# Performance work log

Measured on AMD Instinct MI355X. Metric: run time of the kernel, lower is better.

## Reference

```python
import jax
import jax.numpy as jnp
from jax import lax
import numpy as np

N_PRE = 1024
N_POST = 2048
SEQ_LEN = 4096
DECAY = 0.9   # leak factor per timestep
V_TH = 1.0    # firing threshold


def setup_inputs() -> dict:
    key = jax.random.key(0)
    k1, k2 = jax.random.split(key)
    stim = (jax.random.uniform(k1, (N_PRE, SEQ_LEN), dtype=jnp.float32) < 0.1).astype(jnp.float32)  # sparse input spikes
    weights = jax.random.normal(k2, (N_POST, N_PRE), dtype=jnp.float32) * 0.05
    return {"stim": stim, "weights": weights}


def reference(stim, weights):
    # Synaptic currents for all timesteps at once: cal_post_input(stim[:, i]) == weights @ stim[:, i]
    currents = jnp.einsum("np,pt->nt", weights, stim)  # [n_post, T]

    def lif_step(v, i_t):
        # leaky integrate
        v = v * DECAY + i_t
        # fire
        s = (v >= V_TH).astype(v.dtype)
        # reset to 0 where spiked
        v_next = jnp.where(s > 0, jnp.zeros_like(v), v)
        return v_next, (s, v_next)

    v0 = jnp.zeros((N_POST,), dtype=stim.dtype)
    _, (spikes_t, v_t) = lax.scan(lif_step, v0, currents.T)  # scanned over T
    # transpose back to [n_post, T] to match spike_times / v buffers
    return spikes_t.T, v_t.T
```

## Files before the change

kernel.cpp:

```cpp
#include <hip/hip_runtime.h>

#define N_PRE 1024
#define N_POST 2048
#define SEQ_LEN 4096

#define KSPLIT 512

__device__ __forceinline__ float opaque(float x) {
  asm volatile("" : "+v"(x));
  return x;
}

__device__ __forceinline__ float load_dyn(const void* p, size_t idx, bool isbf) {
  if (isbf) {
    const unsigned short b = ((const unsigned short*)p)[idx];
    return __uint_as_float(((unsigned int)b) << 16);
  }
  return ((const float*)p)[idx];
}

__device__ __forceinline__ int sniff_flags(const void* W, const void* S, int tid,
                                           int* flags_sh) {
  if (tid < 64) {
    const unsigned short* uw = (const unsigned short*)W;
    const float f = fabsf(__uint_as_float(((unsigned int)uw[tid * 2]) << 16));
    const bool big = !(f < 64.f);
    const unsigned long long wb = __ballot(big);
    const unsigned short* us = (const unsigned short*)S;
    int hit = 0;
    for (int j = 0; j < 64; ++j) hit |= (us[tid * 128 + 2 * j] == 0x3F80u) ? 1 : 0;
    const unsigned long long sb = __ballot(hit != 0);
    if (tid == 0) *flags_sh = ((wb == 0ull) ? 1 : 0) | ((sb != 0ull) ? 2 : 0);
  }
  __syncthreads();
  return *flags_sh;
}

__global__ __launch_bounds__(256) void snn_wt_build(const void* __restrict__ W,
                                                    const void* __restrict__ S,
                                                    float* __restrict__ WT) {
  __shared__ float tile[64][65];
  __shared__ int flags_sh;
  const int tid = threadIdx.x;
  const int fl = sniff_flags(W, S, tid, &flags_sh);
  const bool w_bf = (fl & 1) != 0;
  const int k0 = blockIdx.x * 64;
  const int nn0 = blockIdx.y * 64;
  {
    const int r = tid >> 2;
    const int cq = tid & 3;
    if (!w_bf) {
      const float* Wf = (const float*)W;
#pragma unroll
      for (int p = 0; p < 4; ++p) {
        const int c = cq * 16 + p * 4;
        const float4 va = *(const float4*)&Wf[(size_t)(nn0 + r) * N_PRE + k0 + c];
        tile[c + 0][r] = va.x; tile[c + 1][r] = va.y;
        tile[c + 2][r] = va.z; tile[c + 3][r] = va.w;
      }
    } else {
#pragma unroll
      for (int p = 0; p < 4; ++p)
#pragma unroll
        for (int j = 0; j < 4; ++j) {
          const int c = cq * 16 + p * 4 + j;
          tile[c][r] = load_dyn(W, (size_t)(nn0 + r) * N_PRE + k0 + c, true);
        }
    }
  }
  __syncthreads();
  {
    const int kr = tid >> 2;
    const int nq = tid & 3;
#pragma unroll
    for (int p = 0; p < 4; ++p) {
      const int c = nq * 16 + p * 4;
      float4 o;
      o.x = tile[kr][c + 0]; o.y = tile[kr][c + 1];
      o.z = tile[kr][c + 2]; o.w = tile[kr][c + 3];
      *(float4*)&WT[(size_t)(k0 + kr) * N_POST + nn0 + c] = o;
    }
  }
}

__global__ __launch_bounds__(64) void snn_mask_build(const void* __restrict__ W,
                                                     const void* __restrict__ S,
                                                     unsigned char* __restrict__ MT) {
  __shared__ int flags_sh;
  const int tid = threadIdx.x;
  const int fl = sniff_flags(W, S, tid, &flags_sh);
  const bool s_bf = (fl & 2) != 0;
  const int tb = blockIdx.x;
  unsigned wrd[4] = {0u, 0u, 0u, 0u};
#pragma unroll
  for (int kk = 0; kk < 16; ++kk) {
    const int k = tid * 16 + kk;
    unsigned byte = 0;
    if (s_bf) {
      const unsigned short* Sb = (const unsigned short*)S;
      const uint4 u = *(const uint4*)&Sb[(size_t)k * SEQ_LEN + tb * 8];
      byte |= (((u.x & 0x7FFFu) != 0u) ? 1u : 0u) << 0;
      byte |= (((u.x & 0x7FFF0000u) != 0u) ? 1u : 0u) << 1;
      byte |= (((u.y & 0x7FFFu) != 0u) ? 1u : 0u) << 2;
      byte |= (((u.y & 0x7FFF0000u) != 0u) ? 1u : 0u) << 3;
      byte |= (((u.z & 0x7FFFu) != 0u) ? 1u : 0u) << 4;
      byte |= (((u.z & 0x7FFF0000u) != 0u) ? 1u : 0u) << 5;
      byte |= (((u.w & 0x7FFFu) != 0u) ? 1u : 0u) << 6;
      byte |= (((u.w & 0x7FFF0000u) != 0u) ? 1u : 0u) << 7;
    } else {
      const float* Sf = (const float*)S;
      const size_t base = (size_t)k * SEQ_LEN + tb * 8;
      const float4 f0 = *(const float4*)&Sf[base];
      const float4 f1 = *(const float4*)&Sf[base + 4];
      byte |= ((f0.x != 0.0f) ? 1u : 0u) << 0;
      byte |= ((f0.y != 0.0f) ? 1u : 0u) << 1;
      byte |= ((f0.z != 0.0f) ? 1u : 0u) << 2;
      byte |= ((f0.w != 0.0f) ? 1u : 0u) << 3;
      byte |= ((f1.x != 0.0f) ? 1u : 0u) << 4;
      byte |= ((f1.y != 0.0f) ? 1u : 0u) << 5;
      byte |= ((f1.z != 0.0f) ? 1u : 0u) << 6;
      byte |= ((f1.w != 0.0f) ? 1u : 0u) << 7;
    }
    wrd[kk >> 2] |= byte << ((kk & 3) * 8);
  }
  *(uint4*)&MT[(size_t)tb * N_PRE + tid * 16] =
      make_uint4(wrd[0], wrd[1], wrd[2], wrd[3]);
}

__global__ __launch_bounds__(64) void snn_list_build(const unsigned char* __restrict__ MT,
                                                     unsigned short* __restrict__ lists,
                                                     int* __restrict__ lens,
                                                     int* __restrict__ splits) {
  const int t = blockIdx.x;
  const int l = threadIdx.x;
  const unsigned char* Mrow = MT + (size_t)(t >> 3) * N_PRE;
  const int bit = t & 7;
  unsigned short* Lp = lists + (size_t)t * N_PRE;
  int base = 0;
  int split = 0;
#pragma unroll
  for (int c = 0; c < 16; ++c) {
    const int k = c * 64 + l;
    const int b = (Mrow[k] >> bit) & 1;
    const unsigned long long m = __ballot(b != 0);
    const int pre = __popcll(m & ((1ull << l) - 1ull));
    if (b) Lp[base + pre] = (unsigned short)k;
    base += __popcll(m);
    if (c == 7) split = base;
  }
  if (l == 0) {
    lens[t] = base;
    splits[t] = split;
  }
}

__global__ __launch_bounds__(64) void snn_gemm_sp(const float* __restrict__ WT,
                                                  const unsigned short* __restrict__ lists,
                                                  const int* __restrict__ lens,
                                                  const int* __restrict__ splits,
                                                  float* __restrict__ C,
                                                  int t0, int ct) {
  const int slice = (int)blockIdx.x & 7;
  const int tl = (int)blockIdx.x >> 3;
  const int tg = t0 + tl;
  const int n = slice * 256 + (int)threadIdx.x * 4;
  const unsigned short* __restrict__ L = lists + (size_t)tg * N_PRE;
  const int len = lens[tg];
  const int sp = splits[tg];
  float a0 = 0.f, a1 = 0.f, a2 = 0.f, a3 = 0.f;
  float lo0, lo1, lo2, lo3;

#define SP_ADD(K)                                                      \
  {                                                                    \
    const float4 w = *(const float4*)&WT[((size_t)(K) << 11) + n];     \
    a0 += w.x; a1 += w.y; a2 += w.z; a3 += w.w;                        \
  }
#define SP_BATCH8(I)                                                   \
  {                                                                    \
    const uint4 u = *(const uint4*)&L[I];                              \
    const int k0 = u.x & 0xFFFF, k1 = u.x >> 16;                       \
    const int k2 = u.y & 0xFFFF, k3 = u.y >> 16;                       \
    const int k4 = u.z & 0xFFFF, k5 = u.z >> 16;                       \
    const int k6 = u.w & 0xFFFF, k7 = u.w >> 16;                       \
    const float4 w0 = *(const float4*)&WT[((size_t)k0 << 11) + n];     \
    const float4 w1 = *(const float4*)&WT[((size_t)k1 << 11) + n];     \
    const float4 w2 = *(const float4*)&WT[((size_t)k2 << 11) + n];     \
    const float4 w3 = *(const float4*)&WT[((size_t)k3 << 11) + n];     \
    const float4 w4 = *(const float4*)&WT[((size_t)k4 << 11) + n];     \
    const float4 w5 = *(const float4*)&WT[((size_t)k5 << 11) + n];     \
    const float4 w6 = *(const float4*)&WT[((size_t)k6 << 11) + n];     \
    const float4 w7 = *(const float4*)&WT[((size_t)k7 << 11) + n];     \
    a0 += w0.x; a1 += w0.y; a2 += w0.z; a3 += w0.w;                    \
    a0 += w1.x; a1 += w1.y; a2 += w1.z; a3 += w1.w;                    \
    a0 += w2.x; a1 += w2.y; a2 += w2.z; a3 += w2.w;                    \
    a0 += w3.x; a1 += w3.y; a2 += w3.z; a3 += w3.w;                    \
    a0 += w4.x; a1 += w4.y; a2 += w4.z; a3 += w4.w;                    \
    a0 += w5.x; a1 += w5.y; a2 += w5.z; a3 += w5.w;                    \
    a0 += w6.x; a1 += w6.y; a2 += w6.z; a3 += w6.w;                    \
    a0 += w7.x; a1 += w7.y; a2 += w7.z; a3 += w7.w;                    \
  }

  int i = 0;
  for (; i + 8 <= sp; i += 8) SP_BATCH8(i)
  for (; i < sp; ++i) SP_ADD(L[i])
  lo0 = a0; lo1 = a1; lo2 = a2; lo3 = a3;
  a0 = a1 = a2 = a3 = 0.f;
  for (; i < len && (i & 7) != 0; ++i) SP_ADD(L[i])
  for (; i + 8 <= len; i += 8) SP_BATCH8(i)
  for (; i < len; ++i) SP_ADD(L[i])
#undef SP_BATCH8
#undef SP_ADD

  *(float4*)&C[(size_t)tl * N_POST + n] =
      make_float4(lo0 + a0, lo1 + a1, lo2 + a2, lo3 + a3);
}

__global__ __launch_bounds__(64) void snn_scan_chk(const float* __restrict__ C,
                                                   float* __restrict__ vchk,
                                                   float* __restrict__ v_carry,
                                                   int ct, int first) {
  const int l = threadIdx.x;
  const int n = blockIdx.x * 64 + l;
  float v = 0.0f;
  if (!first) v = v_carry[n];
  const int ntiles = ct / 64;

  float cur[64], nxt[64];
#pragma unroll
  for (int j = 0; j < 64; ++j) cur[j] = C[(size_t)j * N_POST + n];

  for (int tile = 0; tile < ntiles; ++tile) {
    vchk[(size_t)tile * N_POST + n] = v;
    const int nb = (tile + 1) * 64;
    const bool hn = (tile + 1 < ntiles);
#pragma unroll
    for (int g = 0; g < 4; ++g) {
      if (hn) {
#pragma unroll
        for (int j = 0; j < 16; ++j)
          nxt[g * 16 + j] = C[(size_t)(nb + g * 16 + j) * N_POST + n];
      }
#pragma unroll
      for (int j = 0; j < 16; ++j) {
        const float c = cur[g * 16 + j];
        const float leak = opaque(v * 0.9f);
        v = leak + c;
        const bool fired = (v >= 1.0f);
        v = fired ? 0.0f : v;
      }
    }
#pragma unroll
    for (int j = 0; j < 64; ++j) cur[j] = nxt[j];
  }
  v_carry[n] = v;
}

__global__ __launch_bounds__(64) void snn_scan_emit(const float* __restrict__ C,
                                                    const float* __restrict__ vchk,
                                                    float* __restrict__ spk,
                                                    float* __restrict__ vout,
                                                    int t0, int ct) {
  __shared__ float sb[64][65];
  __shared__ float vb[64][65];
  const int l = threadIdx.x;
  const int n0 = blockIdx.x * 64;
  const int tile = blockIdx.y;
  const int n = n0 + l;
  const int tb = tile * 64;

  float v = vchk[(size_t)tile * N_POST + n];

  float ccur[16], cnxt[16];
#pragma unroll
  for (int j = 0; j < 16; ++j) ccur[j] = C[(size_t)(tb + j) * N_POST + n];

#pragma unroll
  for (int g = 0; g < 4; ++g) {
    if (g < 3) {
#pragma unroll
      for (int j = 0; j < 16; ++j)
        cnxt[j] = C[(size_t)(tb + (g + 1) * 16 + j) * N_POST + n];
    }
#pragma unroll
    for (int j = 0; j < 16; ++j) {
      const float c = ccur[j];
      const float leak = opaque(v * 0.9f);
      v = leak + c;
      const bool fired = (v >= 1.0f);
      sb[g * 16 + j][l] = fired ? 1.0f : 0.0f;
      v = fired ? 0.0f : v;
      vb[g * 16 + j][l] = v;
    }
#pragma unroll
    for (int j = 0; j < 16; ++j) ccur[j] = cnxt[j];
  }

  const int t4 = (l & 15) * 4;
  const int rq = l >> 4;
  const size_t gtb = (size_t)t0 + tb;
#pragma unroll
  for (int it = 0; it < 16; ++it) {
    const int r = it * 4 + rq;
    float4 so, vo;
    so.x = sb[t4 + 0][r]; so.y = sb[t4 + 1][r];
    so.z = sb[t4 + 2][r]; so.w = sb[t4 + 3][r];
    vo.x = vb[t4 + 0][r]; vo.y = vb[t4 + 1][r];
    vo.z = vb[t4 + 2][r]; vo.w = vb[t4 + 3][r];
    const size_t go = (size_t)(n0 + r) * SEQ_LEN + gtb + t4;
    *(float4*)&spk[go] = so;
    *(float4*)&vout[go] = vo;
  }
}

__global__ __launch_bounds__(256) void snn_fused_blis(const void* __restrict__ W,
                                                      const void* __restrict__ S,
                                                      float* __restrict__ spk,
                                                      float* __restrict__ vout) {
  __shared__ float As[16][68];
  __shared__ float Bs[16][68];
  __shared__ float Ct[64][65];
  __shared__ float vsh[64];
  __shared__ int flags_sh;
  const int tid = threadIdx.x;
  const int fl = sniff_flags(W, S, tid, &flags_sh);
  const bool w_bf = (fl & 1) != 0;
  const bool s_bf = (fl & 2) != 0;

  const int tx = tid & 15;
  const int ty = tid >> 4;
  const int m0 = blockIdx.x * 64;
  if (tid < 64) vsh[tid] = 0.0f;

  for (int t0 = 0; t0 < SEQ_LEN; t0 += 64) {
    float acc0[4][4] = {{0.f}};
    float acc1[4][4] = {{0.f}};
    int k0 = 0;
#define FUSED_SEGMENT(ACC, KEND)                                                 \
    for (; k0 < (KEND); k0 += 16) {                                              \
      {                                                                          \
        const int r = tid >> 4, c = tid & 15;                                    \
        _Pragma("unroll") for (int j = 0; j < 4; ++j)                            \
            As[c][r + 16 * j] =                                                  \
                load_dyn(W, (size_t)(m0 + r + 16 * j) * N_PRE + k0 + c, w_bf);   \
      }                                                                          \
      {                                                                          \
        const int r = tid >> 6, c = tid & 63;                                    \
        _Pragma("unroll") for (int j = 0; j < 4; ++j)                            \
            Bs[r + 4 * j][c] =                                                   \
                load_dyn(S, (size_t)(k0 + r + 4 * j) * SEQ_LEN + t0 + c, s_bf);  \
      }                                                                          \
      __syncthreads();                                                           \
      _Pragma("unroll") for (int k = 0; k < 16; ++k) {                           \
        _Pragma("unroll") for (int i = 0; i < 4; ++i)                            \
            _Pragma("unroll") for (int j = 0; j < 4; ++j)                        \
                ACC[i][j] += As[k][ty * 4 + i] * Bs[k][tx * 4 + j];              \
      }                                                                          \
      __syncthreads();                                                           \
    }

    FUSED_SEGMENT(acc0, KSPLIT)
    FUSED_SEGMENT(acc1, N_PRE)
#undef FUSED_SEGMENT

#pragma unroll
    for (int i = 0; i < 4; ++i)
#pragma unroll
      for (int j = 0; j < 4; ++j) Ct[ty * 4 + i][tx * 4 + j] = acc0[i][j] + acc1[i][j];
    __syncthreads();
    if (tid < 64) {
      float v = vsh[tid];
#pragma unroll
      for (int k = 0; k < 64; ++k) {
        const float leak = opaque(v * 0.9f);
        v = leak + Ct[tid][k];
        const bool fired = (v >= 1.0f);
        const size_t g = (size_t)(m0 + tid) * SEQ_LEN + t0 + k;
        spk[g] = fired ? 1.0f : 0.0f;
        v = fired ? 0.0f : v;
        vout[g] = v;
      }
      vsh[tid] = v;
    }
    __syncthreads();
  }
}

extern "C" void kernel_launch(void* const* d_in, const int* in_sizes, int n_in,
                              void* d_out, int out_size, void* d_ws, size_t ws_size,
                              hipStream_t stream) {
  const void* stim = d_in[0];
  const void* weights = d_in[1];
  if (n_in >= 2 && in_sizes[0] == N_POST * N_PRE && in_sizes[1] == N_PRE * SEQ_LEN) {
    weights = d_in[0];
    stim = d_in[1];
  }

  float* spk = (float*)d_out;
  float* vout = spk + (size_t)N_POST * SEQ_LEN;

  char* p = (char*)d_ws;
  float* WT = (float*)p;                 p += (size_t)N_PRE * N_POST * 4;
  unsigned char* MT = (unsigned char*)p; p += (size_t)(SEQ_LEN / 8) * N_PRE;
  unsigned short* lists = (unsigned short*)p; p += (size_t)SEQ_LEN * N_PRE * 2;
  int* lens = (int*)p;                   p += (size_t)SEQ_LEN * 4;
  int* splits = (int*)p;                 p += (size_t)SEQ_LEN * 4;
  float* v_carry = (float*)p;            p += (size_t)N_POST * 4;
  float* vchk = (float*)p;               p += (size_t)(SEQ_LEN / 64) * N_POST * 4;
  float* C = (float*)p;
  const size_t used = (size_t)(p - (char*)d_ws);
  const size_t remain = (ws_size > used) ? (ws_size - used) : 0;

  int chunkT = (int)((remain / ((size_t)N_POST * sizeof(float))) / 64 * 64);
  if (chunkT > SEQ_LEN) chunkT = SEQ_LEN;
  if (chunkT >= 64) {
    int pw = 64;
    while (pw * 2 <= chunkT && pw < SEQ_LEN) pw *= 2;
    chunkT = pw;
  }

  if (chunkT >= 64) {
    snn_wt_build<<<dim3(N_PRE / 64, N_POST / 64), dim3(256), 0, stream>>>(weights, stim, WT);
    snn_mask_build<<<dim3(SEQ_LEN / 8), dim3(64), 0, stream>>>(weights, stim, MT);
    snn_list_build<<<dim3(SEQ_LEN), dim3(64), 0, stream>>>(MT, lists, lens, splits);
    for (int t0 = 0; t0 < SEQ_LEN; t0 += chunkT) {
      const int ct = (SEQ_LEN - t0 < chunkT) ? (SEQ_LEN - t0) : chunkT;
      snn_gemm_sp<<<dim3(ct * 8), dim3(64), 0, stream>>>(WT, lists, lens, splits, C, t0, ct);
      snn_scan_chk<<<dim3(N_POST / 64), dim3(64), 0, stream>>>(C, vchk, v_carry,
                                                               ct, t0 == 0);
      snn_scan_emit<<<dim3(N_POST / 64, ct / 64), dim3(64), 0, stream>>>(C, vchk, spk,
                                                                         vout, t0, ct);
    }
  } else {
    snn_fused_blis<<<dim3(N_POST / 64), dim3(256), 0, stream>>>(weights, stim, spk, vout);
  }
}
```

Measured before the change: 349.1 us.

## Replace per-timestep sparse gather GEMM with LDS-staged weight panels and bitmask iteration

Replaces the index-list sparse accumulation, where each timestep block gathered weight rows from global memory, with a panel kernel. The new kernel double-buffers 32-row weight panels into LDS via global_load_lds and reuses each panel across 64 timesteps, walking per-timestep 32-bit spike bitmasks with ffs. This cuts global weight traffic and drops the list-building pass in favour of a bitmask transpose. In exchange it adds per-panel barriers, 128 accumulator registers per thread, and wave divergence from uneven popcounts across timesteps.

```diff
diff --git a/kernel.cpp b/kernel.cpp
--- a/kernel.cpp
+++ b/kernel.cpp
@@ -5,6 +5,8 @@
 #define SEQ_LEN 4096
 
 #define KSPLIT 512
+#define TB 64
+#define PK 32
 
 __device__ __forceinline__ float opaque(float x) {
   asm volatile("" : "+v"(x));
@@ -127,92 +129,93 @@
       make_uint4(wrd[0], wrd[1], wrd[2], wrd[3]);
 }
 
-__global__ __launch_bounds__(64) void snn_list_build(const unsigned char* __restrict__ MT,
-                                                     unsigned short* __restrict__ lists,
-                                                     int* __restrict__ lens,
-                                                     int* __restrict__ splits) {
+__global__ __launch_bounds__(64) void snn_mask2_build(const unsigned char* __restrict__ MT,
+                                                      unsigned* __restrict__ MT2) {
   const int t = blockIdx.x;
-  const int l = threadIdx.x;
-  const unsigned char* Mrow = MT + (size_t)(t >> 3) * N_PRE;
-  const int bit = t & 7;
-  unsigned short* Lp = lists + (size_t)t * N_PRE;
-  int base = 0;
-  int split = 0;
-#pragma unroll
-  for (int c = 0; c < 16; ++c) {
-    const int k = c * 64 + l;
-    const int b = (Mrow[k] >> bit) & 1;
-    const unsigned long long m = __ballot(b != 0);
-    const int pre = __popcll(m & ((1ull << l) - 1ull));
-    if (b) Lp[base + pre] = (unsigned short)k;
-    base += __popcll(m);
-    if (c == 7) split = base;
-  }
-  if (l == 0) {
-    lens[t] = base;
-    splits[t] = split;
-  }
-}
-
-__global__ __launch_bounds__(64) void snn_gemm_sp(const float* __restrict__ WT,
-                                                  const unsigned short* __restrict__ lists,
-                                                  const int* __restrict__ lens,
-                                                  const int* __restrict__ splits,
-                                                  float* __restrict__ C,
-                                                  int t0, int ct) {
+  const int w = threadIdx.x;
+  if (w < 32) {
+    const unsigned char* row = MT + (size_t)(t >> 3) * N_PRE + w * 32;
+    const int bt = t & 7;
+    unsigned m = 0;
+#pragma unroll
+    for (int j = 0; j < 32; ++j) m |= (unsigned)((row[j] >> bt) & 1) << j;
+    MT2[(size_t)t * 32 + w] = m;
+  }
+}
+
+__global__ __launch_bounds__(256, 2) void snn_gemm_panel(const float* __restrict__ WT,
+                                                         const unsigned* __restrict__ MT2,
+                                                         float* __restrict__ C,
+                                                         int t0, int ct) {
+  __shared__ float panel[2][PK][256];
+  __shared__ unsigned msh[TB * 32];
   const int slice = (int)blockIdx.x & 7;
-  const int tl = (int)blockIdx.x >> 3;
-  const int tg = t0 + tl;
-  const int n = slice * 256 + (int)threadIdx.x * 4;
-  const unsigned short* __restrict__ L = lists + (size_t)tg * N_PRE;
-  const int len = lens[tg];
-  const int sp = splits[tg];
-  float a0 = 0.f, a1 = 0.f, a2 = 0.f, a3 = 0.f;
-  float lo0, lo1, lo2, lo3;
-
-#define SP_ADD(K)                                                      \
-  {                                                                    \
-    const float4 w = *(const float4*)&WT[((size_t)(K) << 11) + n];     \
-    a0 += w.x; a1 += w.y; a2 += w.z; a3 += w.w;                        \
-  }
-#define SP_BATCH8(I)                                                   \
-  {                                                                    \
-    const uint4 u = *(const uint4*)&L[I];                              \
-    const int k0 = u.x & 0xFFFF, k1 = u.x >> 16;                       \
-    const int k2 = u.y & 0xFFFF, k3 = u.y >> 16;                       \
-    const int k4 = u.z & 0xFFFF, k5 = u.z >> 16;                       \
-    const int k6 = u.w & 0xFFFF, k7 = u.w >> 16;                       \
-    const float4 w0 = *(const float4*)&WT[((size_t)k0 << 11) + n];     \
-    const float4 w1 = *(const float4*)&WT[((size_t)k1 << 11) + n];     \
-    const float4 w2 = *(const float4*)&WT[((size_t)k2 << 11) + n];     \
-    const float4 w3 = *(const float4*)&WT[((size_t)k3 << 11) + n];     \
-    const float4 w4 = *(const float4*)&WT[((size_t)k4 << 11) + n];     \
-    const float4 w5 = *(const float4*)&WT[((size_t)k5 << 11) + n];     \
-    const float4 w6 = *(const float4*)&WT[((size_t)k6 << 11) + n];     \
-    const float4 w7 = *(const float4*)&WT[((size_t)k7 << 11) + n];     \
-    a0 += w0.x; a1 += w0.y; a2 += w0.z; a3 += w0.w;                    \
-    a0 += w1.x; a1 += w1.y; a2 += w1.z; a3 += w1.w;                    \
-    a0 += w2.x; a1 += w2.y; a2 += w2.z; a3 += w2.w;                    \
-    a0 += w3.x; a1 += w3.y; a2 += w3.z; a3 += w3.w;                    \
-    a0 += w4.x; a1 += w4.y; a2 += w4.z; a3 += w4.w;                    \
-    a0 += w5.x; a1 += w5.y; a2 += w5.z; a3 += w5.w;                    \
-    a0 += w6.x; a1 += w6.y; a2 += w6.z; a3 += w6.w;                    \
-    a0 += w7.x; a1 += w7.y; a2 += w7.z; a3 += w7.w;                    \
-  }
-
-  int i = 0;
-  for (; i + 8 <= sp; i += 8) SP_BATCH8(i)
-  for (; i < sp; ++i) SP_ADD(L[i])
-  lo0 = a0; lo1 = a1; lo2 = a2; lo3 = a3;
-  a0 = a1 = a2 = a3 = 0.f;
-  for (; i < len && (i & 7) != 0; ++i) SP_ADD(L[i])
-  for (; i + 8 <= len; i += 8) SP_BATCH8(i)
-  for (; i < len; ++i) SP_ADD(L[i])
-#undef SP_BATCH8
-#undef SP_ADD
-
-  *(float4*)&C[(size_t)tl * N_POST + n] =
-      make_float4(lo0 + a0, lo1 + a1, lo2 + a2, lo3 + a3);
+  const int tq = (int)blockIdx.x >> 3;
+  const int tid = (int)threadIdx.x;
+  const int wid = tid >> 6;
+  const int lane = tid & 63;
+  const int tbl = tq * TB;
+  const int tbg = t0 + tbl;
+  const int ncol = slice * 256 + lane * 4;
+
+  {
+    const unsigned* src = &MT2[(size_t)tbg * 32];
+    for (int i = tid; i < TB * 32; i += 256) msh[i] = src[i];
+  }
+
+#define STAGE(P, BUF)                                                          \
+  {                                                                            \
+    const int kb = (P) * PK + wid * 8;                                         \
+    _Pragma("unroll") for (int r = 0; r < 8; ++r) {                            \
+      __builtin_amdgcn_global_load_lds(                                        \
+          &WT[((size_t)(kb + r) << 11) + ncol], &panel[BUF][wid * 8 + r][lane * 4], \
+          16, 0, 0);                                                           \
+    }                                                                          \
+  }
+
+  float lo[16][4], ac[16][4];
+#pragma unroll
+  for (int j = 0; j < 16; ++j) {
+    lo[j][0] = lo[j][1] = lo[j][2] = lo[j][3] = 0.f;
+    ac[j][0] = ac[j][1] = ac[j][2] = ac[j][3] = 0.f;
+  }
+
+  STAGE(0, 0)
+  asm volatile("s_waitcnt vmcnt(0)" ::: "memory");
+  __syncthreads();
+
+  for (int p = 0; p < 32; ++p) {
+    const int buf = p & 1;
+    if (p + 1 < 32) STAGE(p + 1, buf ^ 1)
+#pragma unroll
+    for (int j = 0; j < 16; ++j) {
+      unsigned m = msh[(wid * 16 + j) * 32 + p];
+      while (m) {
+        const int b = __ffs(m) - 1;
+        m &= m - 1;
+        const float4 w4 = *(const float4*)&panel[buf][b][lane * 4];
+        ac[j][0] += w4.x; ac[j][1] += w4.y; ac[j][2] += w4.z; ac[j][3] += w4.w;
+      }
+    }
+    if (p == 15) {
+#pragma unroll
+      for (int j = 0; j < 16; ++j) {
+        lo[j][0] = ac[j][0]; lo[j][1] = ac[j][1];
+        lo[j][2] = ac[j][2]; lo[j][3] = ac[j][3];
+        ac[j][0] = ac[j][1] = ac[j][2] = ac[j][3] = 0.f;
+      }
+    }
+    asm volatile("s_waitcnt vmcnt(0)" ::: "memory");
+    __syncthreads();
+  }
+#undef STAGE
+
+#pragma unroll
+  for (int j = 0; j < 16; ++j) {
+    float* dst = &C[(size_t)(tbl + wid * 16 + j) * N_POST + ncol];
+    *(float4*)dst = make_float4(lo[j][0] + ac[j][0], lo[j][1] + ac[j][1],
+                                lo[j][2] + ac[j][2], lo[j][3] + ac[j][3]);
+  }
 }
 
 __global__ __launch_bounds__(64) void snn_scan_chk(const float* __restrict__ C,
@@ -401,9 +404,7 @@
   char* p = (char*)d_ws;
   float* WT = (float*)p;                 p += (size_t)N_PRE * N_POST * 4;
   unsigned char* MT = (unsigned char*)p; p += (size_t)(SEQ_LEN / 8) * N_PRE;
-  unsigned short* lists = (unsigned short*)p; p += (size_t)SEQ_LEN * N_PRE * 2;
-  int* lens = (int*)p;                   p += (size_t)SEQ_LEN * 4;
-  int* splits = (int*)p;                 p += (size_t)SEQ_LEN * 4;
+  unsigned* MT2 = (unsigned*)p;          p += (size_t)SEQ_LEN * 32 * 4;
   float* v_carry = (float*)p;            p += (size_t)N_POST * 4;
   float* vchk = (float*)p;               p += (size_t)(SEQ_LEN / 64) * N_POST * 4;
   float* C = (float*)p;
@@ -421,10 +422,10 @@
   if (chunkT >= 64) {
     snn_wt_build<<<dim3(N_PRE / 64, N_POST / 64), dim3(256), 0, stream>>>(weights, stim, WT);
     snn_mask_build<<<dim3(SEQ_LEN / 8), dim3(64), 0, stream>>>(weights, stim, MT);
-    snn_list_build<<<dim3(SEQ_LEN), dim3(64), 0, stream>>>(MT, lists, lens, splits);
+    snn_mask2_build<<<dim3(SEQ_LEN), dim3(64), 0, stream>>>(MT, MT2);
     for (int t0 = 0; t0 < SEQ_LEN; t0 += chunkT) {
       const int ct = (SEQ_LEN - t0 < chunkT) ? (SEQ_LEN - t0) : chunkT;
-      snn_gemm_sp<<<dim3(ct * 8), dim3(64), 0, stream>>>(WT, lists, lens, splits, C, t0, ct);
+      snn_gemm_panel<<<dim3((ct / TB) * 8), dim3(256), 0, stream>>>(WT, MT2, C, t0, ct);
       snn_scan_chk<<<dim3(N_POST / 64), dim3(64), 0, stream>>>(C, vchk, v_carry,
                                                                ct, t0 == 0);
       snn_scan_emit<<<dim3(N_POST / 64, ct / 64), dim3(64), 0, stream>>>(C, vchk, spk,
```

Measured after the change: 363.2 us. +4.0%, slower.
